# Optimization experiments

Hardware: AMD Instinct MI355X
Metric: run time of the kernel (lower is better)

## Reference

```python
import jax, jax.numpy as jnp
import numpy as np

N = 8192   # nodes per graph batch
D = 128    # node_feat_dim
E = 131072 # edges per graph batch
B = 64     # graphs per batch


def _linear_init(k, fin, fout):
    s = 1.0 / np.sqrt(fin)
    kw, kb = jax.random.split(k)
    W = jax.random.uniform(kw, (fin, fout), jnp.float32, -s, s)
    b = jax.random.uniform(kb, (fout,), jnp.float32, -s, s)
    return W, b


def setup_inputs() -> dict:
    key = jax.random.key(0)
    ks = jax.random.split(key, 10)
    x1 = jax.random.normal(ks[0], (N, D), jnp.float32)
    x2 = jax.random.normal(ks[1], (N, D), jnp.float32)
    edge_index1 = jax.random.randint(ks[2], (2, E), 0, N)
    edge_index2 = jax.random.randint(ks[3], (2, E), 0, N)
    # block-contiguous graph ids; every graph id present on both sides
    batch = jnp.arange(N, dtype=jnp.int32) // (N // B)
    mW1, mb1 = _linear_init(ks[4], 2 * D, 512)
    mW2, mb2 = _linear_init(ks[5], 512, 256)  # 256 == 2*D (update_net constraint)
    uW1, ub1 = _linear_init(ks[6], 4 * D, 512)
    uW2, ub2 = _linear_init(ks[7], 512, 256)
    uW3, ub3 = _linear_init(ks[8], 256, D)
    return dict(x1=x1, edge_index1=edge_index1, batch1=batch,
                x2=x2, edge_index2=edge_index2, batch2=batch,
                mW1=mW1, mb1=mb1, mW2=mW2, mb2=mb2,
                uW1=uW1, ub1=ub1, uW2=uW2, ub2=ub2, uW3=uW3, ub3=ub3)


def _message_aggr(x, edge_index, mW1, mb1, mW2, mb2):
    tgt, src = edge_index[0], edge_index[1]
    inp = jnp.concatenate([x[src], x[tgt]], axis=-1)          # [E, 2D]
    msg = jax.nn.relu(inp @ mW1 + mb1) @ mW2 + mb2            # [E, 2D]
    return jax.ops.segment_sum(msg, tgt, num_segments=x.shape[0])


def _cross_attention(x1, batch1, x2, batch2):
    scores = x1 @ x2.T                                        # [N1, N2]
    mask = batch1[:, None] == batch2[None, :]
    scores = jnp.where(mask, scores, -jnp.inf)
    att1 = x1 - jax.nn.softmax(scores, axis=1) @ x2
    att2 = x2 - jax.nn.softmax(scores, axis=0).T @ x1
    return att1, att2


def _node_update(x, messages, attentions, uW1, ub1, uW2, ub2, uW3, ub3):
    u = jnp.concatenate([messages, attentions, x], axis=-1)   # [N, 4D]
    h = jax.nn.relu(u @ uW1 + ub1)
    h = jax.nn.relu(h @ uW2 + ub2)
    return x + h @ uW3 + ub3                                  # residual update


def reference(x1, edge_index1, batch1, x2, edge_index2, batch2,
              mW1, mb1, mW2, mb2, uW1, ub1, uW2, ub2, uW3, ub3):
    m1 = _message_aggr(x1, edge_index1, mW1, mb1, mW2, mb2)
    m2 = _message_aggr(x2, edge_index2, mW1, mb1, mW2, mb2)
    a1, a2 = _cross_attention(x1, batch1, x2, batch2)
    new_x1 = _node_update(x1, m1, a1, uW1, ub1, uW2, ub2, uW3, ub3)
    new_x2 = _node_update(x2, m2, a2, uW1, ub1, uW2, ub2, uW3, ub3)
    return new_x1, new_x2
```

## Files before the change

kernel.cpp:

```cpp
#include <hip/hip_runtime.h>
#include <stdint.h>


typedef unsigned short u16;
typedef __bf16 bf16x8 __attribute__((ext_vector_type(8)));
typedef float f32x4 __attribute__((ext_vector_type(4)));

#define NN 8192
#define DD 128
#define EE 131072
#define GS 128
#define NG 64

__device__ __forceinline__ float bf2f(u16 u){
  return __uint_as_float(((uint32_t)u) << 16);
}
__device__ __forceinline__ u16 f2bf(float f){
  uint32_t x = __float_as_uint(f);
  return (u16)((x + 0x7fffu + ((x >> 16) & 1u)) >> 16);
}
__device__ __forceinline__ void gload16(const u16* g, u16* l){
  __builtin_amdgcn_global_load_lds(
      (const __attribute__((address_space(1))) uint32_t*)(uintptr_t)g,
      (__attribute__((address_space(3))) uint32_t*)(uintptr_t)l, 16, 0, 0);
}
template<int N>
__device__ __forceinline__ void wbar(){
  if constexpr (N == 0)      asm volatile("s_waitcnt vmcnt(0)" ::: "memory");
  else if constexpr (N == 1) asm volatile("s_waitcnt vmcnt(1)" ::: "memory");
  else if constexpr (N == 2) asm volatile("s_waitcnt vmcnt(2)" ::: "memory");
  else if constexpr (N == 4) asm volatile("s_waitcnt vmcnt(4)" ::: "memory");
  __builtin_amdgcn_s_barrier();
  __builtin_amdgcn_sched_barrier(0);
}
__device__ __forceinline__ void bar(){
  __builtin_amdgcn_s_barrier();
  __builtin_amdgcn_sched_barrier(0);
}

template<bool DEGBIAS, typename OT>
__device__ __forceinline__ void gemm_body(
    const u16* __restrict__ A, int lda,
    const u16* __restrict__ Wt, const float* __restrict__ bias,
    const int* __restrict__ deg,
    OT* __restrict__ out, int ldc, int K, int bx, int by,
    u16* __restrict__ sh, int t)
{
  u16* As0 = sh;         u16* Bs0 = sh + 4096;
  u16* As1 = sh + 8192;  u16* Bs1 = sh + 12288;
  const int brow = by << 7, bcol = bx << 7;
  const int w = t >> 6, lane = t & 63;
  const int rb = (w >> 1) << 6, cb = (w & 1) << 6;
  const int lr = lane & 15, lq = lane >> 4;

  f32x4 acc[4][4];
  #pragma unroll
  for (int i = 0; i < 4; i++)
    #pragma unroll
    for (int j = 0; j < 4; j++) acc[i][j] = (f32x4){0.f, 0.f, 0.f, 0.f};

  const int s0 = t, s1 = t + 256;
  const int sw0 = (((s0 & 3) ^ ((s0 >> 2) & 3)) << 3);
  const int sw1 = (((s1 & 3) ^ ((s1 >> 2) & 3)) << 3);
  const u16* Ag0 = A  + (size_t)(brow + (s0 >> 2)) * lda + sw0;
  const u16* Ag1 = A  + (size_t)(brow + (s1 >> 2)) * lda + sw1;
  const u16* Bg0 = Wt + (size_t)(bcol + (s0 >> 2)) * K   + sw0;
  const u16* Bg1 = Wt + (size_t)(bcol + (s1 >> 2)) * K   + sw1;
  const int d0 = s0 << 3, d1 = s1 << 3;

  auto stage = [&](int kb, u16* Al, u16* Bl){
    gload16(Ag0 + kb, Al + d0);
    gload16(Ag1 + kb, Al + d1);
    gload16(Bg0 + kb, Bl + d0);
    gload16(Bg1 + kb, Bl + d1);
  };
  const int swr = ((lq ^ (lr & 3)) << 3);
  auto compute = [&](const u16* Asb, const u16* Bsb){
    bf16x8 af[4], bfr[4];
    #pragma unroll
    for (int mi = 0; mi < 4; mi++)
      af[mi] = *(const bf16x8*)&Asb[(rb + mi * 16 + lr) * 32 + swr];
    #pragma unroll
    for (int ni = 0; ni < 4; ni++)
      bfr[ni] = *(const bf16x8*)&Bsb[(cb + ni * 16 + lr) * 32 + swr];
    #pragma unroll
    for (int mi = 0; mi < 4; mi++)
      #pragma unroll
      for (int ni = 0; ni < 4; ni++)
        acc[mi][ni] = __builtin_amdgcn_mfma_f32_16x16x32_bf16(af[mi], bfr[ni], acc[mi][ni], 0, 0, 0);
  };

  stage(0, As0, Bs0);
  const int half = K >> 6;
  for (int i2 = 0; i2 < half; i2++){
    const int kb = i2 << 6;
    stage(kb + 32, As1, Bs1);
    wbar<4>();
    compute(As0, Bs0);
    bar();
    if (i2 + 1 < half){
      stage(kb + 64, As0, Bs0);
      wbar<4>();
    } else {
      wbar<0>();
    }
    compute(As1, Bs1);
    bar();
  }

  #pragma unroll
  for (int mi = 0; mi < 4; mi++)
    #pragma unroll
    for (int ni = 0; ni < 4; ni++)
      #pragma unroll
      for (int rr = 0; rr < 4; rr++){
        int grow = brow + rb + mi * 16 + lq * 4 + rr;
        int gcol = bcol + cb + ni * 16 + lr;
        float v = acc[mi][ni][rr];
        if (bias) v += DEGBIAS ? (float)deg[grow] * bias[gcol] : bias[gcol];
        out[(size_t)grow * ldc + gcol] = (OT)f2bf(v);
      }
}

__device__ __forceinline__ void pq_gemm(
    const u16* __restrict__ A, const u16* __restrict__ Wt,
    const float* __restrict__ bias, u16* __restrict__ out,
    int bx, int by, u16* __restrict__ sh, int t)
{
  u16* As = sh;
  u16* Bs = sh + 16384;
  const int brow = by << 7, bcol = bx << 7;
  const int w = t >> 6, lane = t & 63;
  const int rb = (w >> 1) << 6, cb = (w & 1) << 6;
  const int lr = lane & 15, lq = lane >> 4;

  #pragma unroll
  for (int i = 0; i < 8; i++){
    int sg = i * 256 + t;
    int r = sg >> 4, p = sg & 15;
    int l = p ^ (r & 7);
    gload16(A  + (size_t)(brow + r) * 128 + (l << 3), As + sg * 8);
    gload16(Wt + (size_t)(bcol + r) * 128 + (l << 3), Bs + sg * 8);
  }
  wbar<0>();

  f32x4 acc[4][4];
  #pragma unroll
  for (int i = 0; i < 4; i++)
    #pragma unroll
    for (int j = 0; j < 4; j++) acc[i][j] = (f32x4){0.f, 0.f, 0.f, 0.f};

  #pragma unroll
  for (int kb = 0; kb < 4; kb++){
    bf16x8 af[4], bfr[4];
    #pragma unroll
    for (int mi = 0; mi < 4; mi++){
      int row = rb + mi * 16 + lr;
      af[mi] = *(const bf16x8*)&As[(row << 7) + ((((kb << 2) | lq) ^ (row & 7)) << 3)];
    }
    #pragma unroll
    for (int ni = 0; ni < 4; ni++){
      int row = cb + ni * 16 + lr;
      bfr[ni] = *(const bf16x8*)&Bs[(row << 7) + ((((kb << 2) | lq) ^ (row & 7)) << 3)];
    }
    #pragma unroll
    for (int mi = 0; mi < 4; mi++)
      #pragma unroll
      for (int ni = 0; ni < 4; ni++)
        acc[mi][ni] = __builtin_amdgcn_mfma_f32_16x16x32_bf16(af[mi], bfr[ni], acc[mi][ni], 0, 0, 0);
  }

  #pragma unroll
  for (int mi = 0; mi < 4; mi++)
    #pragma unroll
    for (int ni = 0; ni < 4; ni++)
      #pragma unroll
      for (int rr = 0; rr < 4; rr++){
        int grow = brow + rb + mi * 16 + lq * 4 + rr;
        int gcol = bcol + cb + ni * 16 + lr;
        out[(size_t)grow * 1024 + gcol] = f2bf(acc[mi][ni][rr] + bias[gcol]);
      }
}

__global__ __launch_bounds__(256)
void pre_k(const float* __restrict__ mW1, const float* __restrict__ mb1,
           const float* __restrict__ mW2, const float* __restrict__ uW1,
           const float* __restrict__ uW2, const float* __restrict__ uW3,
           const float* __restrict__ x1, const float* __restrict__ x2,
           const int* __restrict__ ei1, const int* __restrict__ ei2,
           u16* __restrict__ WtPQ, float* __restrict__ bPQ,
           u16* __restrict__ Wtm2, u16* __restrict__ Wtu1,
           u16* __restrict__ Wtu2, u16* __restrict__ Wtu3,
           u16* __restrict__ xb, u16* __restrict__ xt,
           u16* __restrict__ U, int* __restrict__ deg)
{
  __shared__ u16 T[8704];
  int b = blockIdx.x, t = threadIdx.x;
  if (b < 2692){
    if (b < 512){
      int idx = b * 256 + t; int c = idx >> 7, k = idx & 127;
      int row = (c < 512) ? k : 128 + k;
      WtPQ[idx] = f2bf(mW1[(size_t)row * 512 + (c & 511)]);
    } else if (b < 1024){
      int idx = (b - 512) * 256 + t; int c = idx >> 9, k = idx & 511;
      Wtm2[idx] = f2bf(mW2[(size_t)k * 256 + c]);
    } else if (b < 2048){
      int idx = (b - 1024) * 256 + t; int c = idx >> 9, k = idx & 511;
      Wtu1[idx] = f2bf(uW1[(size_t)k * 512 + c]);
    } else if (b < 2560){
      int idx = (b - 2048) * 256 + t; int c = idx >> 9, k = idx & 511;
      Wtu2[idx] = f2bf(uW2[(size_t)k * 256 + c]);
    } else if (b < 2688){
      int idx = (b - 2560) * 256 + t; int c = idx >> 8, k = idx & 255;
      Wtu3[idx] = f2bf(uW3[(size_t)k * 128 + c]);
    } else {
      int idx = (b - 2688) * 256 + t;
      bPQ[idx] = (idx < 512) ? 0.f : mb1[idx - 512];
    }
  } else if (b < 4740){
    int a = b - 2692;
    int side = a >> 10, blk = a & 1023;
    const float* x = side ? x2 : x1;
    int i4 = blk * 256 + t;
    float4 v = *(const float4*)&x[(size_t)i4 * 4];
    uint2 pk;
    pk.x = (uint32_t)f2bf(v.x) | ((uint32_t)f2bf(v.y) << 16);
    pk.y = (uint32_t)f2bf(v.z) | ((uint32_t)f2bf(v.w) << 16);
    *(uint2*)&xb[(size_t)side * NN * DD + (size_t)i4 * 4] = pk;
    int n = i4 >> 5, d = (i4 << 2) & 127;
    *(uint2*)&U[((size_t)side * NN + n) * 512 + 384 + d] = pk;
  } else if (b < 4996){
    int a = b - 4740;
    int side = a >> 7, blk = a & 127;
    const float* x = side ? x2 : x1;
    u16* dst = xt + (size_t)side * DD * NN;
    const int n0 = blk * 64;
    #pragma unroll
    for (int i = 0; i < 8; i++){
      int s = i * 256 + t;
      int r = s >> 5, c4 = (s & 31) << 2;
      float4 v = *(const float4*)&x[(size_t)(n0 + r) * DD + c4];
      uint2 pk;
      pk.x = (uint32_t)f2bf(v.x) | ((uint32_t)f2bf(v.y) << 16);
      pk.y = (uint32_t)f2bf(v.z) | ((uint32_t)f2bf(v.w) << 16);
      *(uint2*)&T[r * 136 + c4] = pk;
    }
    __syncthreads();
    #pragma unroll
    for (int i = 0; i < 8; i++){
      int s = i * 256 + t;
      int d = s >> 4, n4 = (s & 15) << 2;
      uint32_t a0 = T[(n4 + 0) * 136 + d];
      uint32_t a1 = T[(n4 + 1) * 136 + d];
      uint32_t a2 = T[(n4 + 2) * 136 + d];
      uint32_t a3 = T[(n4 + 3) * 136 + d];
      uint2 pk; pk.x = a0 | (a1 << 16); pk.y = a2 | (a3 << 16);
      *(uint2*)(dst + (size_t)d * NN + n0 + n4) = pk;
    }
  } else {
    int a = b - 4996;
    int side = a >> 9, blk = a & 511;
    const int* ei = side ? ei2 : ei1;
    int e = blk * 256 + t;
    atomicAdd(&deg[side * NN + ei[e]], 1);
  }
}

__global__ __launch_bounds__(256)
void scan_k(const int* __restrict__ deg,
            int* __restrict__ offs1, int* __restrict__ cur1,
            int* __restrict__ offs2, int* __restrict__ cur2){
  const int* d = deg + blockIdx.x * NN;
  int* offs = blockIdx.x ? offs2 : offs1;
  int* cur  = blockIdx.x ? cur2  : cur1;
  __shared__ int part[256];
  const int t = threadIdx.x;
  const int base = t * 32;
  int loc[32];
  int s = 0;
  #pragma unroll
  for (int i = 0; i < 32; i++){ loc[i] = s; s += d[base + i]; }
  part[t] = s;
  __syncthreads();
  for (int off = 1; off < 256; off <<= 1){
    int v = (t >= off) ? part[t - off] : 0;
    __syncthreads();
    part[t] += v;
    __syncthreads();
  }
  int pre = (t == 0) ? 0 : part[t - 1];
  #pragma unroll
  for (int i = 0; i < 32; i++){
    int o = pre + loc[i];
    offs[base + i] = o;
    cur[base + i]  = o;
  }
  if (t == 255) offs[NN] = part[255];
}

__global__ __launch_bounds__(256)
void mid_k(const u16* __restrict__ xb, const u16* __restrict__ WtPQ,
           const float* __restrict__ bPQ, u16* __restrict__ PQ,
           const int* __restrict__ ei1, const int* __restrict__ ei2,
           int* __restrict__ cur1, int* __restrict__ cur2,
           int* __restrict__ srt1, int* __restrict__ srt2)
{
  __shared__ u16 sh[32768];
  const int b = blockIdx.x, t = threadIdx.x;
  if (b < 1024){
    pq_gemm(xb, WtPQ, bPQ, PQ, b >> 7, b & 127, sh, t);
  } else {
    int a = b - 1024;
    int side = a >> 9, blk = a & 511;
    const int* ei = side ? ei2 : ei1;
    int* cur = side ? cur2 : cur1;
    int* srt = side ? srt2 : srt1;
    int e = blk * 256 + t;
    int tgt = ei[e], src = ei[EE + e];
    int p = atomicAdd(&cur[tgt], 1);
    srt[p] = src;
  }
}

__global__ __launch_bounds__(256)
void gather_k(const int* __restrict__ offs1, const int* __restrict__ srt1,
              const int* __restrict__ offs2, const int* __restrict__ srt2,
              const u16* __restrict__ PQ, u16* __restrict__ S)
{
  const int side = blockIdx.y;
  const int* offs = side ? offs2 : offs1;
  const int* srt  = side ? srt2  : srt1;
  const u16* base = PQ + (size_t)side * NN * 1024;
  u16* Sb = S + (size_t)side * NN * 512;

  const int node = (blockIdx.x << 2) + (threadIdx.x >> 6);
  const int lane = threadIdx.x & 63;
  const int beg = offs[node], end = offs[node + 1];

  uint4 qv = *(const uint4*)(base + (size_t)node * 1024 + 512 + (lane << 3));
  float q[8];
  {
    uint32_t qw[4] = {qv.x, qv.y, qv.z, qv.w};
    #pragma unroll
    for (int i = 0; i < 4; i++){
      q[i * 2]     = bf2f((u16)(qw[i] & 0xffffu));
      q[i * 2 + 1] = bf2f((u16)(qw[i] >> 16));
    }
  }
  float acc[8] = {0.f,0.f,0.f,0.f,0.f,0.f,0.f,0.f};

  int e = beg;
  for (; e + 7 < end; e += 8){
    int sx[8];
    #pragma unroll
    for (int i = 0; i < 8; i++) sx[i] = srt[e + i];
    uint4 pv[8];
    #pragma unroll
    for (int i = 0; i < 8; i++)
      pv[i] = *(const uint4*)(base + (size_t)sx[i] * 1024 + (lane << 3));
    #pragma unroll
    for (int i = 0; i < 8; i++){
      uint32_t w0[4] = {pv[i].x, pv[i].y, pv[i].z, pv[i].w};
      #pragma unroll
      for (int j = 0; j < 4; j++){
        acc[j*2]   += fmaxf(bf2f((u16)(w0[j] & 0xffffu)) + q[j*2],   0.f);
        acc[j*2+1] += fmaxf(bf2f((u16)(w0[j] >> 16))     + q[j*2+1], 0.f);
      }
    }
  }
  for (; e + 3 < end; e += 4){
    int sx[4];
    #pragma unroll
    for (int i = 0; i < 4; i++) sx[i] = srt[e + i];
    uint4 pv[4];
    #pragma unroll
    for (int i = 0; i < 4; i++)
      pv[i] = *(const uint4*)(base + (size_t)sx[i] * 1024 + (lane << 3));
    #pragma unroll
    for (int i = 0; i < 4; i++){
      uint32_t w0[4] = {pv[i].x, pv[i].y, pv[i].z, pv[i].w};
      #pragma unroll
      for (int j = 0; j < 4; j++){
        acc[j*2]   += fmaxf(bf2f((u16)(w0[j] & 0xffffu)) + q[j*2],   0.f);
        acc[j*2+1] += fmaxf(bf2f((u16)(w0[j] >> 16))     + q[j*2+1], 0.f);
      }
    }
  }
  for (; e < end; e++){
    int sA = srt[e];
    uint4 pA = *(const uint4*)(base + (size_t)sA * 1024 + (lane << 3));
    uint32_t aw[4] = {pA.x, pA.y, pA.z, pA.w};
    #pragma unroll
    for (int i = 0; i < 4; i++){
      acc[i*2]   += fmaxf(bf2f((u16)(aw[i] & 0xffffu)) + q[i*2],   0.f);
      acc[i*2+1] += fmaxf(bf2f((u16)(aw[i] >> 16))     + q[i*2+1], 0.f);
    }
  }
  uint4 pk;
  pk.x = (uint32_t)f2bf(acc[0]) | ((uint32_t)f2bf(acc[1]) << 16);
  pk.y = (uint32_t)f2bf(acc[2]) | ((uint32_t)f2bf(acc[3]) << 16);
  pk.z = (uint32_t)f2bf(acc[4]) | ((uint32_t)f2bf(acc[5]) << 16);
  pk.w = (uint32_t)f2bf(acc[6]) | ((uint32_t)f2bf(acc[7]) << 16);
  *(uint4*)(Sb + (size_t)node * 512 + (lane << 3)) = pk;
}

__global__ __launch_bounds__(256)
void msgattn_k(const u16* __restrict__ S, const u16* __restrict__ Wtm2,
               const float* __restrict__ mb2, const int* __restrict__ deg,
               const u16* __restrict__ xb, const u16* __restrict__ xt,
               u16* __restrict__ U)
{
  __shared__ u16 sh[26112];
  const int b = blockIdx.x, t = threadIdx.x;
  if (b < 256){
    gemm_body<true,u16>(S, 512, Wtm2, mb2, deg,
                        U, 512, 512, b >> 7, b & 127, sh, t);
    return;
  }
  const int a = b - 256;
  const int side = a >> 7;
  const int g = a & 63, h = (a >> 6) & 1;
  const u16* Xa = xb + (size_t)side * NN * DD;
  const u16* Xb = xb + (size_t)(1 - side) * NN * DD;
  const u16* Xt = xt + (size_t)(1 - side) * DD * NN;
  u16* Uside = U + (size_t)side * NN * 512;

  u16* XaS = sh;
  u16* XbS = sh + 8704;

  const int w = t >> 6, lane = t & 63;
  const int lr = lane & 15, lq = lane >> 4;

  {
    const u16* sa = Xa + ((size_t)g * GS + h * 64) * DD;
    #pragma unroll
    for (int i = 0; i < 4; i++){
      int s = i * 256 + t; int r = s >> 4, c8 = (s & 15) << 3;
      *(uint4*)&XaS[r * 136 + c8] = *(const uint4*)(sa + (size_t)r * DD + c8);
    }
    const u16* sb = Xb + (size_t)g * GS * DD;
    #pragma unroll
    for (int i = 0; i < 8; i++){
      int s = i * 256 + t; int r = s >> 4, c8 = (s & 15) << 3;
      *(uint4*)&XbS[r * 136 + c8] = *(const uint4*)(sb + (size_t)r * DD + c8);
    }
  }
  __syncthreads();

  f32x4 sc[8];
  #pragma unroll
  for (int ct = 0; ct < 8; ct++) sc[ct] = (f32x4){0.f, 0.f, 0.f, 0.f};
  #pragma unroll
  for (int kb = 0; kb < 4; kb++){
    bf16x8 aa = *(const bf16x8*)&XaS[(w * 16 + lr) * 136 + kb * 32 + (lq << 3)];
    #pragma unroll
    for (int ct = 0; ct < 8; ct++){
      bf16x8 bb = *(const bf16x8*)&XbS[(ct * 16 + lr) * 136 + kb * 32 + (lq << 3)];
      sc[ct] = __builtin_amdgcn_mfma_f32_16x16x32_bf16(aa, bb, sc[ct], 0, 0, 0);
    }
  }
  float inv[4];
  #pragma unroll
  for (int rr = 0; rr < 4; rr++){
    float m = sc[0][rr];
    #pragma unroll
    for (int ct = 1; ct < 8; ct++) m = fmaxf(m, sc[ct][rr]);
    #pragma unroll
    for (int sh_ = 1; sh_ < 16; sh_ <<= 1) m = fmaxf(m, __shfl_xor(m, sh_, 64));
    float s = 0.f;
    #pragma unroll
    for (int ct = 0; ct < 8; ct++){
      float e = __expf(sc[ct][rr] - m);
      sc[ct][rr] = e; s += e;
    }
    #pragma unroll
    for (int sh_ = 1; sh_ < 16; sh_ <<= 1) s += __shfl_xor(s, sh_, 64);
    inv[rr] = 1.f / s;
  }
  #pragma unroll
  for (int ct = 0; ct < 8; ct++)
    #pragma unroll
    for (int rr = 0; rr < 4; rr++)
      XaS[(w * 16 + lq * 4 + rr) * 136 + ct * 16 + lr] = f2bf(sc[ct][rr] * inv[rr]);
  __syncthreads();

  f32x4 o[8];
  #pragma unroll
  for (int ct = 0; ct < 8; ct++) o[ct] = (f32x4){0.f, 0.f, 0.f, 0.f};
  #pragma unroll
  for (int kb = 0; kb < 4; kb++){
    bf16x8 aa = *(const bf16x8*)&XaS[(w * 16 + lr) * 136 + kb * 32 + (lq << 3)];
    #pragma unroll
    for (int ct = 0; ct < 8; ct++){
      bf16x8 bb = *(const bf16x8*)(Xt + (size_t)(ct * 16 + lr) * NN + g * GS + kb * 32 + (lq << 3));
      o[ct] = __builtin_amdgcn_mfma_f32_16x16x32_bf16(aa, bb, o[ct], 0, 0, 0);
    }
  }
  const u16* XaG = Xa + ((size_t)g * GS + h * 64) * DD;
  #pragma unroll
  for (int ct = 0; ct < 8; ct++)
    #pragma unroll
    for (int rr = 0; rr < 4; rr++){
      int row = w * 16 + lq * 4 + rr, col = ct * 16 + lr;
      float xa = bf2f(XaG[(size_t)row * DD + col]);
      Uside[((size_t)g * GS + h * 64 + row) * 512 + 256 + col] = f2bf(xa - o[ct][rr]);
    }
}

__global__ __launch_bounds__(512)
void upd_k(const u16* __restrict__ U,
           const u16* __restrict__ Wtu1, const float* __restrict__ ub1,
           const u16* __restrict__ Wtu2, const float* __restrict__ ub2,
           const u16* __restrict__ Wtu3, const float* __restrict__ ub3,
           const float* __restrict__ x1, const float* __restrict__ x2,
           float* __restrict__ out)
{
  __shared__ u16 sh[66560];
  u16* H1s  = sh;
  u16* H2s  = sh + 33280;
  u16* Bst0 = sh + 50176;
  u16* Bst1 = sh + 58368;

  const int t = threadIdx.x;
  const int w = t >> 6, lane = t & 63;
  const int wr = w >> 2, wc = w & 3;
  const int lr = lane & 15, lq = lane >> 4;
  const int r0 = blockIdx.x << 6;

  const int sB0 = t, sB1 = t + 512;
  const int cB0 = sB0 >> 2, cB1 = sB1 >> 2;
  const int swB0 = (((sB0 & 3) ^ (cB0 & 3)) << 3);
  const int swB1 = (((sB1 & 3) ^ (cB1 & 3)) << 3);
  const int swr = ((lq ^ (lr & 3)) << 3);

  f32x4 acc[2][4];
  auto zacc = [&](){
    #pragma unroll
    for (int i = 0; i < 2; i++)
      #pragma unroll
      for (int j = 0; j < 4; j++) acc[i][j] = (f32x4){0.f, 0.f, 0.f, 0.f};
  };

  bf16x8 afA[2], afB[2];
  auto ldA = [&](int kb, bf16x8 (&af)[2]){
    #pragma unroll
    for (int mi = 0; mi < 2; mi++)
      af[mi] = *(const bf16x8*)&U[(size_t)(r0 + wr * 32 + mi * 16 + lr) * 512 + kb + (lq << 3)];
  };
  auto compA = [&](const bf16x8 (&af)[2], const u16* Bsb){
    bf16x8 bfv[4];
    #pragma unroll
    for (int ct = 0; ct < 4; ct++)
      bfv[ct] = *(const bf16x8*)&Bsb[(wc * 64 + ct * 16 + lr) * 32 + swr];
    #pragma unroll
    for (int mi = 0; mi < 2; mi++)
      #pragma unroll
      for (int ct = 0; ct < 4; ct++)
        acc[mi][ct] = __builtin_amdgcn_mfma_f32_16x16x32_bf16(af[mi], bfv[ct], acc[mi][ct], 0, 0, 0);
  };
  for (int hN = 0; hN < 2; hN++){
    zacc();
    auto stB = [&](int kb, u16* dst){
      gload16(Wtu1 + (size_t)(hN * 256 + cB0) * 512 + kb + swB0, dst + sB0 * 8);
      gload16(Wtu1 + (size_t)(hN * 256 + cB1) * 512 + kb + swB1, dst + sB1 * 8);
    };
    stB(0, Bst0);
    ldA(0, afA);
    for (int i2 = 0; i2 < 8; i2++){
      const int kb = i2 << 6;
      stB(kb + 32, Bst1); ldA(kb + 32, afB);
      wbar<4>();
      compA(afA, Bst0);
      bar();
      if (i2 < 7){
        stB(kb + 64, Bst0); ldA(kb + 64, afA);
        wbar<4>();
      } else {
        wbar<0>();
      }
      compA(afB, Bst1);
      bar();
    }
    #pragma unroll
    for (int mi = 0; mi < 2; mi++)
      #pragma unroll
      for (int ct = 0; ct < 4; ct++)
        #pragma unroll
        for (int rr = 0; rr < 4; rr++){
          int row = wr * 32 + mi * 16 + lq * 4 + rr;
          int col = wc * 64 + ct * 16 + lr;
          float v = acc[mi][ct][rr] + ub1[hN * 256 + col];
          H1s[row * 520 + hN * 256 + col] = f2bf(fmaxf(v, 0.f));
        }
  }
  __syncthreads();

  zacc();
  {
    auto stB = [&](int kb, u16* dst){
      gload16(Wtu2 + (size_t)cB0 * 512 + kb + swB0, dst + sB0 * 8);
      gload16(Wtu2 + (size_t)cB1 * 512 + kb + swB1, dst + sB1 * 8);
    };
    auto comp = [&](int kb, const u16* Bsb){
      bf16x8 af[2], bfv[4];
      #pragma unroll
      for (int mi = 0; mi < 2; mi++)
        af[mi] = *(const bf16x8*)&H1s[(wr * 32 + mi * 16 + lr) * 520 + kb + (lq << 3)];
      #pragma unroll
      for (int ct = 0; ct < 4; ct++)
        bfv[ct] = *(const bf16x8*)&Bsb[(wc * 64 + ct * 16 + lr) * 32 + swr];
      #pragma unroll
      for (int mi = 0; mi < 2; mi++)
        #pragma unroll
        for (int ct = 0; ct < 4; ct++)
          acc[mi][ct] = __builtin_amdgcn_mfma_f32_16x16x32_bf16(af[mi], bfv[ct], acc[mi][ct], 0, 0, 0);
    };
    stB(0, Bst0);
    for (int i2 = 0; i2 < 8; i2++){
      const int kb = i2 << 6;
      stB(kb + 32, Bst1);
      wbar<2>();
      comp(kb, Bst0);
      bar();
      if (i2 < 7){
        stB(kb + 64, Bst0);
        wbar<2>();
      } else {
        wbar<0>();
      }
      comp(kb + 32, Bst1);
      bar();
    }
    #pragma unroll
    for (int mi = 0; mi < 2; mi++)
      #pragma unroll
      for (int ct = 0; ct < 4; ct++)
        #pragma unroll
        for (int rr = 0; rr < 4; rr++){
          int row = wr * 32 + mi * 16 + lq * 4 + rr;
          int col = wc * 64 + ct * 16 + lr;
          H2s[row * 264 + col] = f2bf(fmaxf(acc[mi][ct][rr] + ub2[col], 0.f));
        }
  }
  __syncthreads();

  zacc();
  {
    auto stB = [&](int kb, u16* dst){
      gload16(Wtu3 + (size_t)cB0 * 256 + kb + swB0, dst + sB0 * 8);
    };
    auto comp = [&](int kb, const u16* Bsb){
      bf16x8 af[2], bfv[2];
      #pragma unroll
      for (int mi = 0; mi < 2; mi++)
        af[mi] = *(const bf16x8*)&H2s[(wr * 32 + mi * 16 + lr) * 264 + kb + (lq << 3)];
      #pragma unroll
      for (int ct = 0; ct < 2; ct++)
        bfv[ct] = *(const bf16x8*)&Bsb[(wc * 32 + ct * 16 + lr) * 32 + swr];
      #pragma unroll
      for (int mi = 0; mi < 2; mi++)
        #pragma unroll
        for (int ct = 0; ct < 2; ct++)
          acc[mi][ct] = __builtin_amdgcn_mfma_f32_16x16x32_bf16(af[mi], bfv[ct], acc[mi][ct], 0, 0, 0);
    };
    stB(0, Bst0);
    for (int i2 = 0; i2 < 4; i2++){
      const int kb = i2 << 6;
      stB(kb + 32, Bst1);
      wbar<1>();
      comp(kb, Bst0);
      bar();
      if (i2 < 3){
        stB(kb + 64, Bst0);
        wbar<1>();
      } else {
        wbar<0>();
      }
      comp(kb + 32, Bst1);
      bar();
    }
    #pragma unroll
    for (int mi = 0; mi < 2; mi++)
      #pragma unroll
      for (int ct = 0; ct < 2; ct++)
        #pragma unroll
        for (int rr = 0; rr < 4; rr++){
          int row = wr * 32 + mi * 16 + lq * 4 + rr;
          int col = wc * 32 + ct * 16 + lr;
          int grow = r0 + row;
          const float* rp = (grow < NN) ? x1 : x2;
          float v = acc[mi][ct][rr] + ub3[col]
                  + rp[(size_t)(grow & (NN - 1)) * 128 + col];
          out[(size_t)grow * 128 + col] = v;
        }
  }
}

extern "C" void kernel_launch(void* const* d_in, const int* in_sizes, int n_in,
                              void* d_out, int out_size, void* d_ws, size_t ws_size,
                              hipStream_t stream)
{
  const float* x1  = (const float*)d_in[0];
  const int*   ei1 = (const int*)  d_in[1];
  const float* x2  = (const float*)d_in[3];
  const int*   ei2 = (const int*)  d_in[4];
  const float* mW1 = (const float*)d_in[6];
  const float* mb1 = (const float*)d_in[7];
  const float* mW2 = (const float*)d_in[8];
  const float* mb2 = (const float*)d_in[9];
  const float* uW1 = (const float*)d_in[10];
  const float* ub1 = (const float*)d_in[11];
  const float* uW2 = (const float*)d_in[12];
  const float* ub2 = (const float*)d_in[13];
  const float* uW3 = (const float*)d_in[14];
  const float* ub3 = (const float*)d_in[15];
  float* out = (float*)d_out;

  char* w = (char*)d_ws;
  auto alloc = [&](size_t b){ char* p = w; w += (b + 255) & ~(size_t)255; return p; };
  u16*  S    = (u16*)alloc((size_t)2 * NN * 512 * 2);
  u16*  PQ   = (u16*)alloc((size_t)2 * NN * 1024 * 2);
  u16*  xb   = (u16*)alloc((size_t)2 * NN * DD * 2);
  u16*  xt   = (u16*)alloc((size_t)2 * DD * NN * 2);
  u16*  U    = (u16*)alloc((size_t)2 * NN * 512 * 2);
  int*  deg  = (int*)alloc((size_t)2 * NN * 4);
  int*  offs1 = (int*)alloc((NN + 1) * 4);
  int*  offs2 = (int*)alloc((NN + 1) * 4);
  int*  cur1  = (int*)alloc(NN * 4);
  int*  cur2  = (int*)alloc(NN * 4);
  int*  srt1  = (int*)alloc((size_t)EE * 4);
  int*  srt2  = (int*)alloc((size_t)EE * 4);
  u16*  WtPQ = (u16*)alloc(1024 * 128 * 2);
  float* bPQ = (float*)alloc(1024 * 4);
  u16*  Wtm2 = (u16*)alloc(256 * 512 * 2);
  u16*  Wtu1 = (u16*)alloc(512 * 512 * 2);
  u16*  Wtu2 = (u16*)alloc(256 * 512 * 2);
  u16*  Wtu3 = (u16*)alloc(128 * 256 * 2);

  hipMemsetAsync(deg, 0, (size_t)2 * NN * 4, stream);

  pre_k<<<4996 + 1024, 256, 0, stream>>>(
      mW1, mb1, mW2, uW1, uW2, uW3, x1, x2, ei1, ei2,
      WtPQ, bPQ, Wtm2, Wtu1, Wtu2, Wtu3, xb, xt, U, deg);

  scan_k<<<2, 256, 0, stream>>>(deg, offs1, cur1, offs2, cur2);

  mid_k<<<2048, 256, 0, stream>>>(xb, WtPQ, bPQ, PQ, ei1, ei2,
                                  cur1, cur2, srt1, srt2);

  gather_k<<<dim3(NN / 4, 2), 256, 0, stream>>>(offs1, srt1, offs2, srt2, PQ, S);

  msgattn_k<<<512, 256, 0, stream>>>(S, Wtm2, mb2, deg, xb, xt, U);

  upd_k<<<256, 512, 0, stream>>>(U, Wtu1, ub1, Wtu2, ub2, Wtu3, ub3,
                                 x1, x2, out);
}
```

Measured before the change: 222.2 us.

## Fold degree scan into last pre_k block and move attention into mid_k

```diff
diff --git a/kernel.cpp b/kernel.cpp
--- a/kernel.cpp
+++ b/kernel.cpp
@@ -192,9 +192,14 @@
            u16* __restrict__ Wtm2, u16* __restrict__ Wtu1,
            u16* __restrict__ Wtu2, u16* __restrict__ Wtu3,
            u16* __restrict__ xb, u16* __restrict__ xt,
-           u16* __restrict__ U, int* __restrict__ deg)
+           u16* __restrict__ U, int* __restrict__ deg,
+           int* __restrict__ done,
+           int* __restrict__ offs1, int* __restrict__ cur1,
+           int* __restrict__ offs2, int* __restrict__ cur2)
 {
   __shared__ u16 T[8704];
+  __shared__ int part[256];
+  __shared__ int lastf;
   int b = blockIdx.x, t = threadIdx.x;
   if (b < 2692){
     if (b < 512){
@@ -263,39 +268,44 @@
     const int* ei = side ? ei2 : ei1;
     int e = blk * 256 + t;
     atomicAdd(&deg[side * NN + ei[e]], 1);
-  }
-}
-
-__global__ __launch_bounds__(256)
-void scan_k(const int* __restrict__ deg,
-            int* __restrict__ offs1, int* __restrict__ cur1,
-            int* __restrict__ offs2, int* __restrict__ cur2){
-  const int* d = deg + blockIdx.x * NN;
-  int* offs = blockIdx.x ? offs2 : offs1;
-  int* cur  = blockIdx.x ? cur2  : cur1;
-  __shared__ int part[256];
-  const int t = threadIdx.x;
-  const int base = t * 32;
-  int loc[32];
-  int s = 0;
-  #pragma unroll
-  for (int i = 0; i < 32; i++){ loc[i] = s; s += d[base + i]; }
-  part[t] = s;
-  __syncthreads();
-  for (int off = 1; off < 256; off <<= 1){
-    int v = (t >= off) ? part[t - off] : 0;
+    __threadfence();
     __syncthreads();
-    part[t] += v;
+    if (t == 0) lastf = (atomicAdd(done, 1) == 1023);
     __syncthreads();
-  }
-  int pre = (t == 0) ? 0 : part[t - 1];
-  #pragma unroll
-  for (int i = 0; i < 32; i++){
-    int o = pre + loc[i];
-    offs[base + i] = o;
-    cur[base + i]  = o;
-  }
-  if (t == 255) offs[NN] = part[255];
+    if (lastf){
+      __threadfence();
+      for (int sd = 0; sd < 2; sd++){
+        const int* d = deg + sd * NN;
+        int* offs = sd ? offs2 : offs1;
+        int* cur  = sd ? cur2  : cur1;
+        const int base = t * 32;
+        int loc[32];
+        int s = 0;
+        #pragma unroll
+        for (int i = 0; i < 32; i++){
+          loc[i] = s;
+          s += __hip_atomic_load(&d[base + i], __ATOMIC_RELAXED, __HIP_MEMORY_SCOPE_AGENT);
+        }
+        part[t] = s;
+        __syncthreads();
+        for (int off = 1; off < 256; off <<= 1){
+          int v = (t >= off) ? part[t - off] : 0;
+          __syncthreads();
+          part[t] += v;
+          __syncthreads();
+        }
+        int pre = (t == 0) ? 0 : part[t - 1];
+        #pragma unroll
+        for (int i = 0; i < 32; i++){
+          int o = pre + loc[i];
+          offs[base + i] = o;
+          cur[base + i]  = o;
+        }
+        if (t == 255) offs[NN] = part[255];
+        __syncthreads();
+      }
+    }
+  }
 }
 
 __global__ __launch_bounds__(256)
@@ -303,13 +313,16 @@
            const float* __restrict__ bPQ, u16* __restrict__ PQ,
            const int* __restrict__ ei1, const int* __restrict__ ei2,
            int* __restrict__ cur1, int* __restrict__ cur2,
-           int* __restrict__ srt1, int* __restrict__ srt2)
+           int* __restrict__ srt1, int* __restrict__ srt2,
+           const u16* __restrict__ xt, u16* __restrict__ U)
 {
   __shared__ u16 sh[32768];
   const int b = blockIdx.x, t = threadIdx.x;
   if (b < 1024){
     pq_gemm(xb, WtPQ, bPQ, PQ, b >> 7, b & 127, sh, t);
-  } else {
+    return;
+  }
+  if (b < 2048){
     int a = b - 1024;
     int side = a >> 9, blk = a & 511;
     const int* ei = side ? ei2 : ei1;
@@ -319,7 +332,96 @@
     int tgt = ei[e], src = ei[EE + e];
     int p = atomicAdd(&cur[tgt], 1);
     srt[p] = src;
-  }
+    return;
+  }
+  const int a = b - 2048;
+  const int side = a >> 7;
+  const int g = a & 63, h = (a >> 6) & 1;
+  const u16* Xa = xb + (size_t)side * NN * DD;
+  const u16* Xb = xb + (size_t)(1 - side) * NN * DD;
+  const u16* Xt = xt + (size_t)(1 - side) * DD * NN;
+  u16* Uside = U + (size_t)side * NN * 512;
+
+  u16* XaS = sh;
+  u16* XbS = sh + 8704;
+
+  const int w = t >> 6, lane = t & 63;
+  const int lr = lane & 15, lq = lane >> 4;
+
+  {
+    const u16* sa = Xa + ((size_t)g * GS + h * 64) * DD;
+    #pragma unroll
+    for (int i = 0; i < 4; i++){
+      int s = i * 256 + t; int r = s >> 4, c8 = (s & 15) << 3;
+      *(uint4*)&XaS[r * 136 + c8] = *(const uint4*)(sa + (size_t)r * DD + c8);
+    }
+    const u16* sb = Xb + (size_t)g * GS * DD;
+    #pragma unroll
+    for (int i = 0; i < 8; i++){
+      int s = i * 256 + t; int r = s >> 4, c8 = (s & 15) << 3;
+      *(uint4*)&XbS[r * 136 + c8] = *(const uint4*)(sb + (size_t)r * DD + c8);
+    }
+  }
+  __syncthreads();
+
+  f32x4 sc[8];
+  #pragma unroll
+  for (int ct = 0; ct < 8; ct++) sc[ct] = (f32x4){0.f, 0.f, 0.f, 0.f};
+  #pragma unroll
+  for (int kb = 0; kb < 4; kb++){
+    bf16x8 aa = *(const bf16x8*)&XaS[(w * 16 + lr) * 136 + kb * 32 + (lq << 3)];
+    #pragma unroll
+    for (int ct = 0; ct < 8; ct++){
+      bf16x8 bb = *(const bf16x8*)&XbS[(ct * 16 + lr) * 136 + kb * 32 + (lq << 3)];
+      sc[ct] = __builtin_amdgcn_mfma_f32_16x16x32_bf16(aa, bb, sc[ct], 0, 0, 0);
+    }
+  }
+  float inv[4];
+  #pragma unroll
+  for (int rr = 0; rr < 4; rr++){
+    float m = sc[0][rr];
+    #pragma unroll
+    for (int ct = 1; ct < 8; ct++) m = fmaxf(m, sc[ct][rr]);
+    #pragma unroll
+    for (int sh_ = 1; sh_ < 16; sh_ <<= 1) m = fmaxf(m, __shfl_xor(m, sh_, 64));
+    float s = 0.f;
+    #pragma unroll
+    for (int ct = 0; ct < 8; ct++){
+      float e = __expf(sc[ct][rr] - m);
+      sc[ct][rr] = e; s += e;
+    }
+    #pragma unroll
+    for (int sh_ = 1; sh_ < 16; sh_ <<= 1) s += __shfl_xor(s, sh_, 64);
+    inv[rr] = 1.f / s;
+  }
+  #pragma unroll
+  for (int ct = 0; ct < 8; ct++)
+    #pragma unroll
+    for (int rr = 0; rr < 4; rr++)
+      XaS[(w * 16 + lq * 4 + rr) * 136 + ct * 16 + lr] = f2bf(sc[ct][rr] * inv[rr]);
+  __syncthreads();
+
+  f32x4 o[8];
+  #pragma unroll
+  for (int ct = 0; ct < 8; ct++) o[ct] = (f32x4){0.f, 0.f, 0.f, 0.f};
+  #pragma unroll
+  for (int kb = 0; kb < 4; kb++){
+    bf16x8 aa = *(const bf16x8*)&XaS[(w * 16 + lr) * 136 + kb * 32 + (lq << 3)];
+    #pragma unroll
+    for (int ct = 0; ct < 8; ct++){
+      bf16x8 bb = *(const bf16x8*)(Xt + (size_t)(ct * 16 + lr) * NN + g * GS + kb * 32 + (lq << 3));
+      o[ct] = __builtin_amdgcn_mfma_f32_16x16x32_bf16(aa, bb, o[ct], 0, 0, 0);
+    }
+  }
+  const u16* XaG = Xa + ((size_t)g * GS + h * 64) * DD;
+  #pragma unroll
+  for (int ct = 0; ct < 8; ct++)
+    #pragma unroll
+    for (int rr = 0; rr < 4; rr++){
+      int row = w * 16 + lq * 4 + rr, col = ct * 16 + lr;
+      float xa = bf2f(XaG[(size_t)row * DD + col]);
+      Uside[((size_t)g * GS + h * 64 + row) * 512 + 256 + col] = f2bf(xa - o[ct][rr]);
+    }
 }
 
 __global__ __launch_bounds__(256)
@@ -405,106 +507,14 @@
 }
 
 __global__ __launch_bounds__(256)
-void msgattn_k(const u16* __restrict__ S, const u16* __restrict__ Wtm2,
-               const float* __restrict__ mb2, const int* __restrict__ deg,
-               const u16* __restrict__ xb, const u16* __restrict__ xt,
-               u16* __restrict__ U)
+void msg_k(const u16* __restrict__ S, const u16* __restrict__ Wtm2,
+           const float* __restrict__ mb2, const int* __restrict__ deg,
+           u16* __restrict__ U)
 {
-  __shared__ u16 sh[26112];
-  const int b = blockIdx.x, t = threadIdx.x;
-  if (b < 256){
-    gemm_body<true,u16>(S, 512, Wtm2, mb2, deg,
-                        U, 512, 512, b >> 7, b & 127, sh, t);
-    return;
-  }
-  const int a = b - 256;
-  const int side = a >> 7;
-  const int g = a & 63, h = (a >> 6) & 1;
-  const u16* Xa = xb + (size_t)side * NN * DD;
-  const u16* Xb = xb + (size_t)(1 - side) * NN * DD;
-  const u16* Xt = xt + (size_t)(1 - side) * DD * NN;
-  u16* Uside = U + (size_t)side * NN * 512;
-
-  u16* XaS = sh;
-  u16* XbS = sh + 8704;
-
-  const int w = t >> 6, lane = t & 63;
-  const int lr = lane & 15, lq = lane >> 4;
-
-  {
-    const u16* sa = Xa + ((size_t)g * GS + h * 64) * DD;
-    #pragma unroll
-    for (int i = 0; i < 4; i++){
-      int s = i * 256 + t; int r = s >> 4, c8 = (s & 15) << 3;
-      *(uint4*)&XaS[r * 136 + c8] = *(const uint4*)(sa + (size_t)r * DD + c8);
-    }
-    const u16* sb = Xb + (size_t)g * GS * DD;
-    #pragma unroll
-    for (int i = 0; i < 8; i++){
-      int s = i * 256 + t; int r = s >> 4, c8 = (s & 15) << 3;
-      *(uint4*)&XbS[r * 136 + c8] = *(const uint4*)(sb + (size_t)r * DD + c8);
-    }
-  }
-  __syncthreads();
-
-  f32x4 sc[8];
-  #pragma unroll
-  for (int ct = 0; ct < 8; ct++) sc[ct] = (f32x4){0.f, 0.f, 0.f, 0.f};
-  #pragma unroll
-  for (int kb = 0; kb < 4; kb++){
-    bf16x8 aa = *(const bf16x8*)&XaS[(w * 16 + lr) * 136 + kb * 32 + (lq << 3)];
-    #pragma unroll
-    for (int ct = 0; ct < 8; ct++){
-      bf16x8 bb = *(const bf16x8*)&XbS[(ct * 16 + lr) * 136 + kb * 32 + (lq << 3)];
-      sc[ct] = __builtin_amdgcn_mfma_f32_16x16x32_bf16(aa, bb, sc[ct], 0, 0, 0);
-    }
-  }
-  float inv[4];
-  #pragma unroll
-  for (int rr = 0; rr < 4; rr++){
-    float m = sc[0][rr];
-    #pragma unroll
-    for (int ct = 1; ct < 8; ct++) m = fmaxf(m, sc[ct][rr]);
-    #pragma unroll
-    for (int sh_ = 1; sh_ < 16; sh_ <<= 1) m = fmaxf(m, __shfl_xor(m, sh_, 64));
-    float s = 0.f;
-    #pragma unroll
-    for (int ct = 0; ct < 8; ct++){
-      float e = __expf(sc[ct][rr] - m);
-      sc[ct][rr] = e; s += e;
-    }
-    #pragma unroll
-    for (int sh_ = 1; sh_ < 16; sh_ <<= 1) s += __shfl_xor(s, sh_, 64);
-    inv[rr] = 1.f / s;
-  }
-  #pragma unroll
-  for (int ct = 0; ct < 8; ct++)
-    #pragma unroll
-    for (int rr = 0; rr < 4; rr++)
-      XaS[(w * 16 + lq * 4 + rr) * 136 + ct * 16 + lr] = f2bf(sc[ct][rr] * inv[rr]);
-  __syncthreads();
-
-  f32x4 o[8];
-  #pragma unroll
-  for (int ct = 0; ct < 8; ct++) o[ct] = (f32x4){0.f, 0.f, 0.f, 0.f};
-  #pragma unroll
-  for (int kb = 0; kb < 4; kb++){
-    bf16x8 aa = *(const bf16x8*)&XaS[(w * 16 + lr) * 136 + kb * 32 + (lq << 3)];
-    #pragma unroll
-    for (int ct = 0; ct < 8; ct++){
-      bf16x8 bb = *(const bf16x8*)(Xt + (size_t)(ct * 16 + lr) * NN + g * GS + kb * 32 + (lq << 3));
-      o[ct] = __builtin_amdgcn_mfma_f32_16x16x32_bf16(aa, bb, o[ct], 0, 0, 0);
-    }
-  }
-  const u16* XaG = Xa + ((size_t)g * GS + h * 64) * DD;
-  #pragma unroll
-  for (int ct = 0; ct < 8; ct++)
-    #pragma unroll
-    for (int rr = 0; rr < 4; rr++){
-      int row = w * 16 + lq * 4 + rr, col = ct * 16 + lr;
-      float xa = bf2f(XaG[(size_t)row * DD + col]);
-      Uside[((size_t)g * GS + h * 64 + row) * 512 + 256 + col] = f2bf(xa - o[ct][rr]);
-    }
+  __shared__ u16 sh[16384];
+  gemm_body<true,u16>(S, 512, Wtm2, mb2, deg,
+                      U, 512, 512, blockIdx.x >> 7, blockIdx.x & 127,
+                      sh, threadIdx.x);
 }
 
 __global__ __launch_bounds__(512)
@@ -724,6 +734,7 @@
   u16*  xt   = (u16*)alloc((size_t)2 * DD * NN * 2);
   u16*  U    = (u16*)alloc((size_t)2 * NN * 512 * 2);
   int*  deg  = (int*)alloc((size_t)2 * NN * 4);
+  int*  done = (int*)alloc(256);
   int*  offs1 = (int*)alloc((NN + 1) * 4);
   int*  offs2 = (int*)alloc((NN + 1) * 4);
   int*  cur1  = (int*)alloc(NN * 4);
@@ -737,20 +748,19 @@
   u16*  Wtu2 = (u16*)alloc(256 * 512 * 2);
   u16*  Wtu3 = (u16*)alloc(128 * 256 * 2);
 
-  hipMemsetAsync(deg, 0, (size_t)2 * NN * 4, stream);
+  hipMemsetAsync(deg, 0, (size_t)2 * NN * 4 + 256, stream);
 
   pre_k<<<4996 + 1024, 256, 0, stream>>>(
       mW1, mb1, mW2, uW1, uW2, uW3, x1, x2, ei1, ei2,
-      WtPQ, bPQ, Wtm2, Wtu1, Wtu2, Wtu3, xb, xt, U, deg);
-
-  scan_k<<<2, 256, 0, stream>>>(deg, offs1, cur1, offs2, cur2);
-
-  mid_k<<<2048, 256, 0, stream>>>(xb, WtPQ, bPQ, PQ, ei1, ei2,
-                                  cur1, cur2, srt1, srt2);
+      WtPQ, bPQ, Wtm2, Wtu1, Wtu2, Wtu3, xb, xt, U, deg, done,
+      offs1, cur1, offs2, cur2);
+
+  mid_k<<<2304, 256, 0, stream>>>(xb, WtPQ, bPQ, PQ, ei1, ei2,
+                                  cur1, cur2, srt1, srt2, xt, U);
 
   gather_k<<<dim3(NN / 4, 2), 256, 0, stream>>>(offs1, srt1, offs2, srt2, PQ, S);
 
-  msgattn_k<<<512, 256, 0, stream>>>(S, Wtm2, mb2, deg, xb, xt, U);
+  msg_k<<<256, 256, 0, stream>>>(S, Wtm2, mb2, deg, U);
 
   upd_k<<<256, 512, 0, stream>>>(U, Wtu1, ub1, Wtu2, ub2, Wtu3, ub3,
                                  x1, x2, out);
```

Result: slower. 317.4 us (+42.8%).
